# Optimization experiments

Hardware: AMD Instinct MI355X
Metric: run time of the kernel (lower is better)

## Reference

```python
import jax, jax.numpy as jnp
import numpy as np

D_MODEL = 1024
NUM_HEADS = 16
D_K = D_MODEL // NUM_HEADS
D_FF = 4096
THETA = 10000.0
EPS = 1e-5
B, S = 4, 2048


def _trunc_normal(key, shape, fan_in, fan_out):
    std = (2.0 / (fan_in + fan_out)) ** 0.5
    return jax.random.truncated_normal(key, -3.0, 3.0, shape, jnp.float32) * std


def setup_inputs() -> dict:
    key = jax.random.key(0)
    ks = jax.random.split(key, 8)
    return {
        "x": jax.random.normal(ks[0], (B, S, D_MODEL), jnp.float32),
        "wq": _trunc_normal(ks[1], (D_MODEL, D_MODEL), D_MODEL, D_MODEL),
        "wk": _trunc_normal(ks[2], (D_MODEL, D_MODEL), D_MODEL, D_MODEL),
        "wv": _trunc_normal(ks[3], (D_MODEL, D_MODEL), D_MODEL, D_MODEL),
        "wo": _trunc_normal(ks[4], (D_MODEL, D_MODEL), D_MODEL, D_MODEL),
        "g1": jnp.ones((D_MODEL,), jnp.float32),
        "g2": jnp.ones((D_MODEL,), jnp.float32),
        "w1": _trunc_normal(ks[5], (D_FF, D_MODEL), D_MODEL, D_FF),
        "w2": _trunc_normal(ks[6], (D_MODEL, D_FF), D_FF, D_MODEL),
        "w3": _trunc_normal(ks[7], (D_FF, D_MODEL), D_MODEL, D_FF),
    }


def _rmsnorm(x, g):
    rms = jnp.sqrt(jnp.mean(x * x, axis=-1, keepdims=True) + EPS)
    return x / rms * g


def _rope(x):
    # x: [b, h, s, d_k], interleaved rotary embedding
    s = x.shape[-2]
    inv_freq = 1.0 / (THETA ** (jnp.arange(0, D_K, 2, dtype=jnp.float32) / D_K))
    angles = jnp.arange(s, dtype=jnp.float32)[:, None] * inv_freq  # [s, d_k/2]
    cos, sin = jnp.cos(angles), jnp.sin(angles)
    x1, x2 = x[..., ::2], x[..., 1::2]
    rot = jnp.stack([x1 * cos - x2 * sin, x1 * sin + x2 * cos], axis=-1)
    return rot.reshape(x.shape)


def reference(x, wq, wk, wv, wo, g1, g2, w1, w2, w3):
    b, s, _ = x.shape
    h, dk = NUM_HEADS, D_K

    # --- attention sublayer ---
    xn = _rmsnorm(x, g1)
    q = (xn @ wq.T).reshape(b, s, h, dk).transpose(0, 2, 1, 3)
    k = (xn @ wk.T).reshape(b, s, h, dk).transpose(0, 2, 1, 3)
    v = (xn @ wv.T).reshape(b, s, h, dk).transpose(0, 2, 1, 3)
    q, k = _rope(q), _rope(k)

    scores = jnp.einsum("bhqd,bhkd->bhqk", q, k) / (dk ** 0.5)
    causal = jnp.tril(jnp.ones((s, s), dtype=bool))
    scores = jnp.where(causal, scores, -1e9)
    attn = jax.nn.softmax(scores, axis=-1)
    ctx = jnp.einsum("bhqk,bhkd->bhqd", attn, v)
    ctx = ctx.transpose(0, 2, 1, 3).reshape(b, s, h * dk)
    y = x + ctx @ wo.T

    # --- SwiGLU FFN sublayer ---
    yn = _rmsnorm(y, g2)
    a = yn @ w1.T
    ff = (a * jax.nn.sigmoid(a)) * (yn @ w3.T)
    return y + ff @ w2.T
```

## Files before the change

### kernel.cpp

```cpp
#include <hip/hip_runtime.h>
#include <hip/hip_bf16.h>

typedef unsigned short u16;
typedef unsigned int u32;
typedef __bf16 bf16_8 __attribute__((ext_vector_type(8)));
typedef float f32x4 __attribute__((ext_vector_type(4)));

#define DEV __device__ __forceinline__

static const int T_TOK = 8192;
static const int DM    = 1024;
static const int SEQ   = 2048;

DEV u16 f2b(float f) {
  union { float f; u32 u; } v; v.f = f;
  u32 r = v.u + 0x7fffu + ((v.u >> 16) & 1u);
  return (u16)(r >> 16);
}
DEV float b2f(u16 b) {
  union { u32 u; float f; } v; v.u = ((u32)b) << 16;
  return v.f;
}
DEV void gload16(void* lds, const void* g) {
  __builtin_amdgcn_global_load_lds((const __attribute__((address_space(1))) u32*)g,
                                   (__attribute__((address_space(3))) u32*)lds, 16, 0, 0);
}
DEV void vmdrain() { asm volatile("s_waitcnt vmcnt(0)" ::: "memory"); }
DEV uint2 tr_read(u32 addr) {
  uint2 r;
  asm volatile("ds_read_b64_tr_b16 %0, %1" : "=v"(r) : "v"(addr));
  return r;
}

__global__ void cvt_bf16(const float* __restrict__ in, u16* __restrict__ out, int n) {
  int i = (blockIdx.x * blockDim.x + threadIdx.x) * 4;
  if (i >= n) return;
  float4 v = *(const float4*)(in + i);
  union { u16 h[4]; uint2 u; } pk;
  pk.h[0] = f2b(v.x); pk.h[1] = f2b(v.y); pk.h[2] = f2b(v.z); pk.h[3] = f2b(v.w);
  *(uint2*)(out + i) = pk.u;
}

__launch_bounds__(256)
__global__ void rmsnorm_k(const float* __restrict__ x, const float* __restrict__ g,
                          u16* __restrict__ out) {
  const int row = blockIdx.x;
  const float4 v = ((const float4*)(x + (size_t)row * DM))[threadIdx.x];
  float ss = v.x*v.x + v.y*v.y + v.z*v.z + v.w*v.w;
  #pragma unroll
  for (int off = 1; off < 64; off <<= 1) ss += __shfl_xor(ss, off, 64);
  __shared__ float ws[4];
  if ((threadIdx.x & 63) == 0) ws[threadIdx.x >> 6] = ss;
  __syncthreads();
  float tot = ws[0] + ws[1] + ws[2] + ws[3];
  float inv = rsqrtf(tot * (1.0f / DM) + 1e-5f);
  const float4 gv = ((const float4*)g)[threadIdx.x];
  union { u16 h[4]; uint2 u; } pk;
  pk.h[0] = f2b(v.x * inv * gv.x);
  pk.h[1] = f2b(v.y * inv * gv.y);
  pk.h[2] = f2b(v.z * inv * gv.z);
  pk.h[3] = f2b(v.w * inv * gv.w);
  *(uint2*)(out + (size_t)row * DM + threadIdx.x * 4) = pk.u;
}

__global__ void rope_k(u16* __restrict__ buf, float scale) {
  int idx = blockIdx.x * blockDim.x + threadIdx.x;
  if (idx >= T_TOK * 512) return;
  int t = idx >> 9;
  int p = idx & 511;
  int d = p & 31;
  int s = t & (SEQ - 1);
  float inv = __expf(-(float)d * (logf(10000.0f) / 32.0f));
  float ang = (float)s * inv;
  float sn = sinf(ang), cs = cosf(ang);
  size_t off = (size_t)t * DM + (size_t)(p >> 5) * 64 + 2 * d;
  float x1 = b2f(buf[off]), x2 = b2f(buf[off + 1]);
  buf[off]     = f2b((x1 * cs - x2 * sn) * scale);
  buf[off + 1] = f2b((x1 * sn + x2 * cs) * scale);
}


#define GEMM_STAGE(As, Bs, Ap, Bp, K)                                          \
  {                                                                            \
    int c = tid;                                                               \
    gload16((char*)As + (size_t)w * 1024,                                      \
            Ap + (size_t)(brow + (c >> 2)) * K + kk + (((c & 3) ^ ((c >> 3) & 3)) << 3)); \
    gload16((char*)Bs + (size_t)w * 1024,                                      \
            Bp + (size_t)(bcol + (c >> 2)) * K + kk + (((c & 3) ^ ((c >> 3) & 3)) << 3)); \
    c = tid + 256;                                                             \
    gload16((char*)As + 4096 + (size_t)w * 1024,                               \
            Ap + (size_t)(brow + (c >> 2)) * K + kk + (((c & 3) ^ ((c >> 3) & 3)) << 3)); \
    gload16((char*)Bs + 4096 + (size_t)w * 1024,                               \
            Bp + (size_t)(bcol + (c >> 2)) * K + kk + (((c & 3) ^ ((c >> 3) & 3)) << 3)); \
  }

#define GEMM_MFMA(As, Bs)                                                      \
  {                                                                            \
    const int swz = ((lr >> 1) & 3) ^ lg;                                      \
    bf16_8 af[4], bfr[4];                                                      \
    _Pragma("unroll")                                                          \
    for (int m = 0; m < 4; ++m)                                                \
      af[m] = *(const bf16_8*)&As[(wr * 64 + m * 16 + lr) * 32 + (swz << 3)];  \
    _Pragma("unroll")                                                          \
    for (int n = 0; n < 4; ++n)                                                \
      bfr[n] = *(const bf16_8*)&Bs[(wc * 64 + n * 16 + lr) * 32 + (swz << 3)]; \
    _Pragma("unroll")                                                          \
    for (int m = 0; m < 4; ++m)                                                \
      _Pragma("unroll")                                                        \
      for (int n = 0; n < 4; ++n)                                              \
        acc[m][n] = __builtin_amdgcn_mfma_f32_16x16x32_bf16(af[m], bfr[n], acc[m][n], 0, 0, 0); \
  }

template<int MODE>
__launch_bounds__(256)
__global__ void gemm_nt(const u16* __restrict__ A, const u16* __restrict__ B,
                        u16* Cb, float* __restrict__ Cf,
                        const float* __restrict__ resid, const u16* aux,
                        int N, int K) {
  __shared__ __attribute__((aligned(16))) u16 As[128 * 32];
  __shared__ __attribute__((aligned(16))) u16 Bs[128 * 32];
  const int tid = threadIdx.x;
  const int w = tid >> 6, l = tid & 63;
  const int wr = w >> 1, wc = w & 1;
  const int nwg = gridDim.x * gridDim.y;
  const int id  = blockIdx.y * gridDim.x + blockIdx.x;
  const int nid = (id & 7) * (nwg >> 3) + (id >> 3);
  const int bx = nid % gridDim.x, by = nid / gridDim.x;
  const int brow = by * 128;
  const int bcol = bx * 128;
  const int lr = l & 15, lg = l >> 4;
  f32x4 acc[4][4] = {};

  for (int kk = 0; kk < K; kk += 32) {
    GEMM_STAGE(As, Bs, A, B, K)
    vmdrain();
    __syncthreads();
    GEMM_MFMA(As, Bs)
    __syncthreads();
  }

  #pragma unroll
  for (int m = 0; m < 4; ++m) {
    #pragma unroll
    for (int n = 0; n < 4; ++n) {
      #pragma unroll
      for (int r = 0; r < 4; ++r) {
        int row = brow + wr * 64 + m * 16 + lg * 4 + r;
        int col = bcol + wc * 64 + n * 16 + lr;
        size_t idx = (size_t)row * N + col;
        float v = acc[m][n][r];
        if (MODE == 0) {
          Cb[idx] = f2b(v);
        } else if (MODE == 1 || MODE == 3) {
          Cf[idx] = resid[idx] + v;
        } else if (MODE == 2) {
          float av = b2f(aux[idx]);
          float sig = 1.0f / (1.0f + __expf(-av));
          Cb[idx] = f2b(av * sig * v);
        }
      }
    }
  }
}

__launch_bounds__(256)
__global__ void gemm_qkv(const u16* __restrict__ A,
                         const u16* __restrict__ Bq, const u16* __restrict__ Bk,
                         const u16* __restrict__ Bv,
                         u16* __restrict__ Oq, u16* __restrict__ Ok,
                         u16* __restrict__ Ov) {
  __shared__ __attribute__((aligned(16))) u16 As[128 * 32];
  __shared__ __attribute__((aligned(16))) u16 Bs[128 * 32];
  const int tid = threadIdx.x;
  const int w = tid >> 6, l = tid & 63;
  const int wr = w >> 1, wc = w & 1;
  const int nwg = gridDim.x * gridDim.y;
  const int id  = blockIdx.y * gridDim.x + blockIdx.x;
  const int nid = (id & 7) * (nwg >> 3) + (id >> 3);
  const int bx = nid % gridDim.x, by = nid / gridDim.x;
  const int brow = by * 128;
  const int mi = bx >> 3;
  const int bcol = (bx & 7) * 128;
  const u16* B = (mi == 0) ? Bq : (mi == 1) ? Bk : Bv;
  u16* O = (mi == 0) ? Oq : (mi == 1) ? Ok : Ov;
  const int lr = l & 15, lg = l >> 4;
  const int K = 1024;
  f32x4 acc[4][4] = {};

  for (int kk = 0; kk < K; kk += 32) {
    GEMM_STAGE(As, Bs, A, B, K)
    vmdrain();
    __syncthreads();
    GEMM_MFMA(As, Bs)
    __syncthreads();
  }

  #pragma unroll
  for (int m = 0; m < 4; ++m)
    #pragma unroll
    for (int n = 0; n < 4; ++n)
      #pragma unroll
      for (int r = 0; r < 4; ++r) {
        int row = brow + wr * 64 + m * 16 + lg * 4 + r;
        int col = bcol + wc * 64 + n * 16 + lr;
        O[(size_t)row * 1024 + col] = f2b(acc[m][n][r]);
      }
}

__launch_bounds__(256)
__global__ void attn_k(const u16* __restrict__ Q, const u16* __restrict__ Kb,
                       const u16* __restrict__ V, u16* __restrict__ CTX) {
  __shared__ __attribute__((aligned(16))) u16 Ks[64 * 64];
  __shared__ __attribute__((aligned(16))) u16 Vs[64 * 64];
  __shared__ __attribute__((aligned(16))) u16 Ps[4][16 * 64];
  const int tid = threadIdx.x, w = tid >> 6, l = tid & 63;
  const int bh = blockIdx.y;
  const int b = bh >> 4, h = bh & 15;
  const int lr = l & 15, lg = l >> 4;
  const size_t base = (size_t)b * SEQ * DM + (size_t)h * 64;
  const u32 vs_base = (u32)(size_t)&Vs[0];

  #pragma unroll 1
  for (int pass = 0; pass < 2; ++pass) {
    const int qt = pass ? (31 - blockIdx.x) : blockIdx.x;
    const int q0 = qt * 64;

    const size_t qrow = base + (size_t)(q0 + w * 16 + lr) * DM;
    bf16_8 qf0 = *(const bf16_8*)&Q[qrow + lg * 8];
    bf16_8 qf1 = *(const bf16_8*)&Q[qrow + 32 + lg * 8];

    f32x4 o[4] = {};
    float mrow[4], lsum[4];
    #pragma unroll
    for (int r = 0; r < 4; ++r) { mrow[r] = -3.0e38f; lsum[r] = 0.0f; }

    for (int kv0 = 0; kv0 < q0 + 64; kv0 += 64) {
      __syncthreads();
      {
        int u = tid, row = u >> 3, slot = u & 7;
        gload16((char*)Ks + (size_t)w * 1024,
                Kb + base + (size_t)(kv0 + row) * DM + ((slot * 8) ^ ((row & 7) << 3)));
        u = tid + 256; row = u >> 3; slot = u & 7;
        gload16((char*)Ks + 4096 + (size_t)w * 1024,
                Kb + base + (size_t)(kv0 + row) * DM + ((slot * 8) ^ ((row & 7) << 3)));
        u = tid;
        int kv = ((u >> 5) << 2) + ((u >> 1) & 3);
        int d  = (((u >> 3) & 3) << 4) + ((u & 1) << 3);
        gload16((char*)Vs + (size_t)w * 1024,
                V + base + (size_t)(kv0 + kv) * DM + d);
        u = tid + 256;
        kv = ((u >> 5) << 2) + ((u >> 1) & 3);
        d  = (((u >> 3) & 3) << 4) + ((u & 1) << 3);
        gload16((char*)Vs + 4096 + (size_t)w * 1024,
                V + base + (size_t)(kv0 + kv) * DM + d);
      }
      vmdrain();
      __syncthreads();

      f32x4 s[4];
      #pragma unroll
      for (int h0 = 0; h0 < 4; ++h0) {
        const int row = h0 * 16 + lr;
        bf16_8 k0 = *(const bf16_8*)&Ks[row * 64 + ((lg * 8) ^ ((lr & 7) << 3))];
        bf16_8 k1 = *(const bf16_8*)&Ks[row * 64 + ((32 + lg * 8) ^ ((lr & 7) << 3))];
        f32x4 z = {};
        z = __builtin_amdgcn_mfma_f32_16x16x32_bf16(qf0, k0, z, 0, 0, 0);
        z = __builtin_amdgcn_mfma_f32_16x16x32_bf16(qf1, k1, z, 0, 0, 0);
        s[h0] = z;
      }

      #pragma unroll
      for (int r = 0; r < 4; ++r) {
        const int qg = q0 + w * 16 + lg * 4 + r;
        #pragma unroll
        for (int h0 = 0; h0 < 4; ++h0) {
          int kg = kv0 + h0 * 16 + lr;
          if (kg > qg) s[h0][r] = -3.0e38f;
        }
        float vmax = fmaxf(fmaxf(s[0][r], s[1][r]), fmaxf(s[2][r], s[3][r]));
        #pragma unroll
        for (int off = 1; off < 16; off <<= 1) vmax = fmaxf(vmax, __shfl_xor(vmax, off, 64));
        float mnew = fmaxf(mrow[r], vmax);
        float alpha = __expf(mrow[r] - mnew);
        mrow[r] = mnew;
        float p[4], rs = 0.0f;
        #pragma unroll
        for (int h0 = 0; h0 < 4; ++h0) { p[h0] = __expf(s[h0][r] - mnew); rs += p[h0]; }
        #pragma unroll
        for (int off = 1; off < 16; off <<= 1) rs += __shfl_xor(rs, off, 64);
        lsum[r] = lsum[r] * alpha + rs;
        o[0][r] *= alpha; o[1][r] *= alpha; o[2][r] *= alpha; o[3][r] *= alpha;
        const int ql = lg * 4 + r;
        #pragma unroll
        for (int h0 = 0; h0 < 4; ++h0)
          Ps[w][ql * 64 + (((h0 * 16 + lr) ^ ((ql & 7) << 3)))] = f2b(p[h0]);
      }

      #pragma unroll
      for (int kc = 0; kc < 2; ++kc) {
        bf16_8 pf = *(const bf16_8*)&Ps[w][lr * 64 + (((kc * 32 + lg * 8) ^ ((lr & 7) << 3)))];
        uint2 t0[4], t1[4];
        #pragma unroll
        for (int n = 0; n < 4; ++n) {
          u32 a0 = vs_base + (u32)((((kc * 8 + lg * 2 + 0) * 4 + n) * 128) + lr * 8);
          u32 a1 = vs_base + (u32)((((kc * 8 + lg * 2 + 1) * 4 + n) * 128) + lr * 8);
          t0[n] = tr_read(a0);
          t1[n] = tr_read(a1);
        }
        asm volatile("s_waitcnt lgkmcnt(0)" ::: "memory");
        __builtin_amdgcn_sched_barrier(0);
        #pragma unroll
        for (int n = 0; n < 4; ++n) {
          union { uint2 u2[2]; bf16_8 v; } vf;
          vf.u2[0] = t0[n]; vf.u2[1] = t1[n];
          o[n] = __builtin_amdgcn_mfma_f32_16x16x32_bf16(pf, vf.v, o[n], 0, 0, 0);
        }
      }
    }

    #pragma unroll
    for (int r = 0; r < 4; ++r) {
      float inv = 1.0f / lsum[r];
      size_t row = (size_t)b * SEQ + q0 + w * 16 + lg * 4 + r;
      #pragma unroll
      for (int n = 0; n < 4; ++n)
        CTX[row * DM + h * 64 + n * 16 + lr] = f2b(o[n][r] * inv);
    }
  }
}

extern "C" void kernel_launch(void* const* d_in, const int* in_sizes, int n_in,
                              void* d_out, int out_size, void* d_ws, size_t ws_size,
                              hipStream_t stream) {
  const float* x  = (const float*)d_in[0];
  const float* wq = (const float*)d_in[1];
  const float* wk = (const float*)d_in[2];
  const float* wv = (const float*)d_in[3];
  const float* wo = (const float*)d_in[4];
  const float* g1 = (const float*)d_in[5];
  const float* g2 = (const float*)d_in[6];
  const float* w1 = (const float*)d_in[7];
  const float* w2 = (const float*)d_in[8];
  const float* w3 = (const float*)d_in[9];

  char* ws = (char*)d_ws;
  const size_t MB = 1024 * 1024;
  u16*  WQb  = (u16*)(ws +  0 * MB);
  u16*  WKb  = (u16*)(ws +  2 * MB);
  u16*  WVb  = (u16*)(ws +  4 * MB);
  u16*  WOb  = (u16*)(ws +  6 * MB);
  u16*  W1b  = (u16*)(ws +  8 * MB);
  u16*  W3b  = (u16*)(ws + 16 * MB);
  u16*  W2b  = (u16*)(ws + 24 * MB);
  u16*  XN   = (u16*)(ws + 32 * MB);
  u16*  Qb   = (u16*)(ws + 48 * MB);
  u16*  Kb   = (u16*)(ws + 64 * MB);
  u16*  Vb   = (u16*)(ws + 80 * MB);
  u16*  CTX  = (u16*)(ws + 96 * MB);
  float* Y   = (float*)(ws + 112 * MB);
  u16*  FFIN = (u16*)(ws + 48 * MB);

  cvt_bf16<<<1024, 256, 0, stream>>>(wq, WQb, 1048576);
  cvt_bf16<<<1024, 256, 0, stream>>>(wk, WKb, 1048576);
  cvt_bf16<<<1024, 256, 0, stream>>>(wv, WVb, 1048576);
  cvt_bf16<<<1024, 256, 0, stream>>>(wo, WOb, 1048576);
  cvt_bf16<<<4096, 256, 0, stream>>>(w1, W1b, 4194304);
  cvt_bf16<<<4096, 256, 0, stream>>>(w3, W3b, 4194304);
  cvt_bf16<<<4096, 256, 0, stream>>>(w2, W2b, 4194304);

  rmsnorm_k<<<T_TOK, 256, 0, stream>>>(x, g1, XN);

  gemm_qkv<<<dim3(24, 64), 256, 0, stream>>>(XN, WQb, WKb, WVb, Qb, Kb, Vb);

  rope_k<<<16384, 256, 0, stream>>>(Qb, 0.125f);
  rope_k<<<16384, 256, 0, stream>>>(Kb, 1.0f);

  attn_k<<<dim3(16, 64), 256, 0, stream>>>(Qb, Kb, Vb, CTX);

  gemm_nt<1><<<dim3(8, 64), 256, 0, stream>>>(CTX, WOb, nullptr, Y, x, nullptr, 1024, 1024);

  rmsnorm_k<<<T_TOK, 256, 0, stream>>>(Y, g2, XN);

  gemm_nt<0><<<dim3(32, 64), 256, 0, stream>>>(XN, W1b, FFIN, nullptr, nullptr, nullptr, 4096, 1024);
  gemm_nt<2><<<dim3(32, 64), 256, 0, stream>>>(XN, W3b, FFIN, nullptr, nullptr, FFIN, 4096, 1024);

  gemm_nt<3><<<dim3(8, 64), 256, 0, stream>>>(FFIN, W2b, nullptr, (float*)d_out, Y, nullptr, 1024, 4096);
}
```

Measured before the change: 750.5 us.

## Double-buffer GEMM and attention LDS tiles and restructure flash-attention softmax

The GEMM and attention kernels now keep two LDS buffers and prefetch the next K tile while computing on the current one, waiting with vmcnt(4) instead of draining all loads. Attention swaps the QK^T MFMA operands so each lane owns one query row, which cuts the row reductions to two shuffles. It also adds a lazy rescale that skips the alpha update when the running max grows by at most 8, and XCD-aware block remapping. The extra LDS halves potential occupancy, and the lazy rescale relies on bounded exponent growth for accuracy.

```diff
diff --git a/kernel.cpp b/kernel.cpp
--- a/kernel.cpp
+++ b/kernel.cpp
@@ -25,12 +25,15 @@
   __builtin_amdgcn_global_load_lds((const __attribute__((address_space(1))) u32*)g,
                                    (__attribute__((address_space(3))) u32*)lds, 16, 0, 0);
 }
-DEV void vmdrain() { asm volatile("s_waitcnt vmcnt(0)" ::: "memory"); }
 DEV uint2 tr_read(u32 addr) {
   uint2 r;
   asm volatile("ds_read_b64_tr_b16 %0, %1" : "=v"(r) : "v"(addr));
   return r;
 }
+#define VMCNT4 asm volatile("s_waitcnt vmcnt(4)" ::: "memory")
+#define VMCNT0 asm volatile("s_waitcnt vmcnt(0)" ::: "memory")
+#define SBAR   __builtin_amdgcn_s_barrier()
+#define SCHED0 __builtin_amdgcn_sched_barrier(0)
 
 __global__ void cvt_bf16(const float* __restrict__ in, u16* __restrict__ out, int n) {
   int i = (blockIdx.x * blockDim.x + threadIdx.x) * 4;
@@ -80,35 +83,49 @@
 }
 
 
-#define GEMM_STAGE(As, Bs, Ap, Bp, K)                                          \
-  {                                                                            \
-    int c = tid;                                                               \
-    gload16((char*)As + (size_t)w * 1024,                                      \
-            Ap + (size_t)(brow + (c >> 2)) * K + kk + (((c & 3) ^ ((c >> 3) & 3)) << 3)); \
-    gload16((char*)Bs + (size_t)w * 1024,                                      \
-            Bp + (size_t)(bcol + (c >> 2)) * K + kk + (((c & 3) ^ ((c >> 3) & 3)) << 3)); \
-    c = tid + 256;                                                             \
-    gload16((char*)As + 4096 + (size_t)w * 1024,                               \
-            Ap + (size_t)(brow + (c >> 2)) * K + kk + (((c & 3) ^ ((c >> 3) & 3)) << 3)); \
-    gload16((char*)Bs + 4096 + (size_t)w * 1024,                               \
-            Bp + (size_t)(bcol + (c >> 2)) * K + kk + (((c & 3) ^ ((c >> 3) & 3)) << 3)); \
-  }
-
-#define GEMM_MFMA(As, Bs)                                                      \
-  {                                                                            \
-    const int swz = ((lr >> 1) & 3) ^ lg;                                      \
-    bf16_8 af[4], bfr[4];                                                      \
-    _Pragma("unroll")                                                          \
-    for (int m = 0; m < 4; ++m)                                                \
-      af[m] = *(const bf16_8*)&As[(wr * 64 + m * 16 + lr) * 32 + (swz << 3)];  \
-    _Pragma("unroll")                                                          \
-    for (int n = 0; n < 4; ++n)                                                \
-      bfr[n] = *(const bf16_8*)&Bs[(wc * 64 + n * 16 + lr) * 32 + (swz << 3)]; \
-    _Pragma("unroll")                                                          \
-    for (int m = 0; m < 4; ++m)                                                \
-      _Pragma("unroll")                                                        \
-      for (int n = 0; n < 4; ++n)                                              \
+#define GEMM_STAGE(d, kk)                                                       \
+  {                                                                             \
+    int c = tid;                                                                \
+    gload16((char*)As + (d) * 8192 + (size_t)w * 1024,                          \
+            A + (size_t)(brow + (c >> 2)) * K + (kk) + (((c & 3) ^ ((c >> 3) & 3)) << 3)); \
+    gload16((char*)Bs + (d) * 8192 + (size_t)w * 1024,                          \
+            B + (size_t)(bcol + (c >> 2)) * K + (kk) + (((c & 3) ^ ((c >> 3) & 3)) << 3)); \
+    c = tid + 256;                                                              \
+    gload16((char*)As + (d) * 8192 + 4096 + (size_t)w * 1024,                   \
+            A + (size_t)(brow + (c >> 2)) * K + (kk) + (((c & 3) ^ ((c >> 3) & 3)) << 3)); \
+    gload16((char*)Bs + (d) * 8192 + 4096 + (size_t)w * 1024,                   \
+            B + (size_t)(bcol + (c >> 2)) * K + (kk) + (((c & 3) ^ ((c >> 3) & 3)) << 3)); \
+  }
+
+#define GEMM_MFMA(d)                                                            \
+  {                                                                             \
+    const u16* Ab = &As[d][0]; const u16* Bb = &Bs[d][0];                       \
+    const int swz = (((lr >> 1) & 3) ^ lg) << 3;                                \
+    bf16_8 af[4], bfr[4];                                                       \
+    _Pragma("unroll")                                                           \
+    for (int m = 0; m < 4; ++m)                                                 \
+      af[m] = *(const bf16_8*)&Ab[(wr * 64 + m * 16 + lr) * 32 + swz];          \
+    _Pragma("unroll")                                                           \
+    for (int n = 0; n < 4; ++n)                                                 \
+      bfr[n] = *(const bf16_8*)&Bb[(wc * 64 + n * 16 + lr) * 32 + swz];         \
+    _Pragma("unroll")                                                           \
+    for (int m = 0; m < 4; ++m)                                                 \
+      _Pragma("unroll")                                                         \
+      for (int n = 0; n < 4; ++n)                                               \
         acc[m][n] = __builtin_amdgcn_mfma_f32_16x16x32_bf16(af[m], bfr[n], acc[m][n], 0, 0, 0); \
+  }
+
+#define GEMM_LOOP                                                               \
+  const int nt = K >> 5;                                                        \
+  GEMM_STAGE(0, 0)                                                              \
+  int cur = 0;                                                                  \
+  for (int t = 0; t < nt; ++t) {                                                \
+    if (t + 1 < nt) { GEMM_STAGE(cur ^ 1, (t + 1) * 32) VMCNT4; }               \
+    else VMCNT0;                                                                \
+    SBAR; SCHED0;                                                               \
+    GEMM_MFMA(cur)                                                              \
+    SCHED0; SBAR;                                                               \
+    cur ^= 1;                                                                   \
   }
 
 template<int MODE>
@@ -117,8 +134,8 @@
                         u16* Cb, float* __restrict__ Cf,
                         const float* __restrict__ resid, const u16* aux,
                         int N, int K) {
-  __shared__ __attribute__((aligned(16))) u16 As[128 * 32];
-  __shared__ __attribute__((aligned(16))) u16 Bs[128 * 32];
+  __shared__ __attribute__((aligned(16))) u16 As[2][128 * 32];
+  __shared__ __attribute__((aligned(16))) u16 Bs[2][128 * 32];
   const int tid = threadIdx.x;
   const int w = tid >> 6, l = tid & 63;
   const int wr = w >> 1, wc = w & 1;
@@ -131,13 +148,7 @@
   const int lr = l & 15, lg = l >> 4;
   f32x4 acc[4][4] = {};
 
-  for (int kk = 0; kk < K; kk += 32) {
-    GEMM_STAGE(As, Bs, A, B, K)
-    vmdrain();
-    __syncthreads();
-    GEMM_MFMA(As, Bs)
-    __syncthreads();
-  }
+  GEMM_LOOP
 
   #pragma unroll
   for (int m = 0; m < 4; ++m) {
@@ -169,8 +180,8 @@
                          const u16* __restrict__ Bv,
                          u16* __restrict__ Oq, u16* __restrict__ Ok,
                          u16* __restrict__ Ov) {
-  __shared__ __attribute__((aligned(16))) u16 As[128 * 32];
-  __shared__ __attribute__((aligned(16))) u16 Bs[128 * 32];
+  __shared__ __attribute__((aligned(16))) u16 As[2][128 * 32];
+  __shared__ __attribute__((aligned(16))) u16 Bs[2][128 * 32];
   const int tid = threadIdx.x;
   const int w = tid >> 6, l = tid & 63;
   const int wr = w >> 1, wc = w & 1;
@@ -187,13 +198,7 @@
   const int K = 1024;
   f32x4 acc[4][4] = {};
 
-  for (int kk = 0; kk < K; kk += 32) {
-    GEMM_STAGE(As, Bs, A, B, K)
-    vmdrain();
-    __syncthreads();
-    GEMM_MFMA(As, Bs)
-    __syncthreads();
-  }
+  GEMM_LOOP
 
   #pragma unroll
   for (int m = 0; m < 4; ++m)
@@ -210,105 +215,134 @@
 __launch_bounds__(256)
 __global__ void attn_k(const u16* __restrict__ Q, const u16* __restrict__ Kb,
                        const u16* __restrict__ V, u16* __restrict__ CTX) {
-  __shared__ __attribute__((aligned(16))) u16 Ks[64 * 64];
-  __shared__ __attribute__((aligned(16))) u16 Vs[64 * 64];
+  __shared__ __attribute__((aligned(16))) u16 Ks[2][64 * 64];
+  __shared__ __attribute__((aligned(16))) u16 Vs[2][64 * 64];
   __shared__ __attribute__((aligned(16))) u16 Ps[4][16 * 64];
   const int tid = threadIdx.x, w = tid >> 6, l = tid & 63;
-  const int bh = blockIdx.y;
+  const int lr = l & 15, lg = l >> 4;
+  const int id = blockIdx.y * gridDim.x + blockIdx.x;
+  const int xcd = id & 7, slot = id >> 3;
+  const int bh = xcd * 8 + (slot >> 4);
+  const int qx = slot & 15;
   const int b = bh >> 4, h = bh & 15;
-  const int lr = l & 15, lg = l >> 4;
   const size_t base = (size_t)b * SEQ * DM + (size_t)h * 64;
-  const u32 vs_base = (u32)(size_t)&Vs[0];
+  const u32 vs0 = (u32)(size_t)&Vs[0][0];
+
+#define ATT_STAGE(d, kv0)                                                       \
+  {                                                                             \
+    int u = tid, row = u >> 3, sl = u & 7;                                      \
+    gload16((char*)Ks + (d) * 8192 + (size_t)w * 1024,                          \
+            Kb + base + (size_t)((kv0) + row) * DM + ((sl * 8) ^ ((row & 7) << 3))); \
+    u = tid + 256; row = u >> 3; sl = u & 7;                                    \
+    gload16((char*)Ks + (d) * 8192 + 4096 + (size_t)w * 1024,                   \
+            Kb + base + (size_t)((kv0) + row) * DM + ((sl * 8) ^ ((row & 7) << 3))); \
+    u = tid;                                                                    \
+    { int kv = ((u >> 5) << 2) + ((u >> 1) & 3);                                \
+      int dd = (((u >> 3) & 3) << 4) + ((u & 1) << 3);                          \
+      gload16((char*)Vs + (d) * 8192 + (size_t)w * 1024,                        \
+              V + base + (size_t)((kv0) + kv) * DM + dd); }                     \
+    u = tid + 256;                                                              \
+    { int kv = ((u >> 5) << 2) + ((u >> 1) & 3);                                \
+      int dd = (((u >> 3) & 3) << 4) + ((u & 1) << 3);                          \
+      gload16((char*)Vs + (d) * 8192 + 4096 + (size_t)w * 1024,                 \
+              V + base + (size_t)((kv0) + kv) * DM + dd); }                     \
+  }
 
   #pragma unroll 1
   for (int pass = 0; pass < 2; ++pass) {
-    const int qt = pass ? (31 - blockIdx.x) : blockIdx.x;
+    const int qt = pass ? (31 - qx) : qx;
     const int q0 = qt * 64;
-
-    const size_t qrow = base + (size_t)(q0 + w * 16 + lr) * DM;
-    bf16_8 qf0 = *(const bf16_8*)&Q[qrow + lg * 8];
-    bf16_8 qf1 = *(const bf16_8*)&Q[qrow + 32 + lg * 8];
+    const int qg = q0 + w * 16 + lr;
+    const size_t qrow = base + (size_t)qg * DM;
+    const bf16_8 qf0 = *(const bf16_8*)&Q[qrow + lg * 8];
+    const bf16_8 qf1 = *(const bf16_8*)&Q[qrow + 32 + lg * 8];
 
     f32x4 o[4] = {};
-    float mrow[4], lsum[4];
-    #pragma unroll
-    for (int r = 0; r < 4; ++r) { mrow[r] = -3.0e38f; lsum[r] = 0.0f; }
-
-    for (int kv0 = 0; kv0 < q0 + 64; kv0 += 64) {
-      __syncthreads();
-      {
-        int u = tid, row = u >> 3, slot = u & 7;
-        gload16((char*)Ks + (size_t)w * 1024,
-                Kb + base + (size_t)(kv0 + row) * DM + ((slot * 8) ^ ((row & 7) << 3)));
-        u = tid + 256; row = u >> 3; slot = u & 7;
-        gload16((char*)Ks + 4096 + (size_t)w * 1024,
-                Kb + base + (size_t)(kv0 + row) * DM + ((slot * 8) ^ ((row & 7) << 3)));
-        u = tid;
-        int kv = ((u >> 5) << 2) + ((u >> 1) & 3);
-        int d  = (((u >> 3) & 3) << 4) + ((u & 1) << 3);
-        gload16((char*)Vs + (size_t)w * 1024,
-                V + base + (size_t)(kv0 + kv) * DM + d);
-        u = tid + 256;
-        kv = ((u >> 5) << 2) + ((u >> 1) & 3);
-        d  = (((u >> 3) & 3) << 4) + ((u & 1) << 3);
-        gload16((char*)Vs + 4096 + (size_t)w * 1024,
-                V + base + (size_t)(kv0 + kv) * DM + d);
-      }
-      vmdrain();
-      __syncthreads();
+    float mr = -3.0e38f, ls = 0.0f;
+    const int nt = qt + 1;
+    ATT_STAGE(0, 0)
+    int cur = 0;
+
+    for (int t = 0; t < nt; ++t) {
+      const int kv0 = t * 64;
+      if (t + 1 < nt) { ATT_STAGE(cur ^ 1, kv0 + 64) VMCNT4; }
+      else VMCNT0;
+      SBAR; SCHED0;
 
       f32x4 s[4];
+      const u16* kbuf = &Ks[cur][0];
       #pragma unroll
       for (int h0 = 0; h0 < 4; ++h0) {
         const int row = h0 * 16 + lr;
-        bf16_8 k0 = *(const bf16_8*)&Ks[row * 64 + ((lg * 8) ^ ((lr & 7) << 3))];
-        bf16_8 k1 = *(const bf16_8*)&Ks[row * 64 + ((32 + lg * 8) ^ ((lr & 7) << 3))];
+        bf16_8 k0 = *(const bf16_8*)&kbuf[row * 64 + ((lg * 8) ^ ((lr & 7) << 3))];
+        bf16_8 k1 = *(const bf16_8*)&kbuf[row * 64 + ((32 + lg * 8) ^ ((lr & 7) << 3))];
         f32x4 z = {};
-        z = __builtin_amdgcn_mfma_f32_16x16x32_bf16(qf0, k0, z, 0, 0, 0);
-        z = __builtin_amdgcn_mfma_f32_16x16x32_bf16(qf1, k1, z, 0, 0, 0);
+        z = __builtin_amdgcn_mfma_f32_16x16x32_bf16(k0, qf0, z, 0, 0, 0);
+        z = __builtin_amdgcn_mfma_f32_16x16x32_bf16(k1, qf1, z, 0, 0, 0);
         s[h0] = z;
       }
 
-      #pragma unroll
-      for (int r = 0; r < 4; ++r) {
-        const int qg = q0 + w * 16 + lg * 4 + r;
+      if (kv0 + 63 > q0 + w * 16) {
         #pragma unroll
         for (int h0 = 0; h0 < 4; ++h0) {
-          int kg = kv0 + h0 * 16 + lr;
-          if (kg > qg) s[h0][r] = -3.0e38f;
+          int kb = kv0 + h0 * 16 + lg * 4;
+          #pragma unroll
+          for (int r = 0; r < 4; ++r)
+            if (kb + r > qg) s[h0][r] = -3.0e38f;
         }
-        float vmax = fmaxf(fmaxf(s[0][r], s[1][r]), fmaxf(s[2][r], s[3][r]));
+      }
+
+      float pm = s[0][0];
+      #pragma unroll
+      for (int h0 = 0; h0 < 4; ++h0)
         #pragma unroll
-        for (int off = 1; off < 16; off <<= 1) vmax = fmaxf(vmax, __shfl_xor(vmax, off, 64));
-        float mnew = fmaxf(mrow[r], vmax);
-        float alpha = __expf(mrow[r] - mnew);
-        mrow[r] = mnew;
-        float p[4], rs = 0.0f;
+        for (int r = 0; r < 4; ++r) pm = fmaxf(pm, s[h0][r]);
+      pm = fmaxf(pm, __shfl_xor(pm, 16, 64));
+      pm = fmaxf(pm, __shfl_xor(pm, 32, 64));
+
+      if (!__all(pm - mr <= 8.0f)) {
+        float mnew = fmaxf(mr, pm);
+        float alpha = __expf(mr - mnew);
+        mr = mnew;
+        ls *= alpha;
         #pragma unroll
-        for (int h0 = 0; h0 < 4; ++h0) { p[h0] = __expf(s[h0][r] - mnew); rs += p[h0]; }
-        #pragma unroll
-        for (int off = 1; off < 16; off <<= 1) rs += __shfl_xor(rs, off, 64);
-        lsum[r] = lsum[r] * alpha + rs;
-        o[0][r] *= alpha; o[1][r] *= alpha; o[2][r] *= alpha; o[3][r] *= alpha;
-        const int ql = lg * 4 + r;
-        #pragma unroll
-        for (int h0 = 0; h0 < 4; ++h0)
-          Ps[w][ql * 64 + (((h0 * 16 + lr) ^ ((ql & 7) << 3)))] = f2b(p[h0]);
-      }
-
+        for (int r = 0; r < 4; ++r) {
+          float ar = __shfl(alpha, lg * 4 + r, 64);
+          o[0][r] *= ar; o[1][r] *= ar; o[2][r] *= ar; o[3][r] *= ar;
+        }
+      }
+
+      float rs = 0.0f;
+      #pragma unroll
+      for (int h0 = 0; h0 < 4; ++h0) {
+        float p0 = __expf(s[h0][0] - mr);
+        float p1 = __expf(s[h0][1] - mr);
+        float p2 = __expf(s[h0][2] - mr);
+        float p3 = __expf(s[h0][3] - mr);
+        rs += (p0 + p1) + (p2 + p3);
+        union { u16 hh[4]; uint2 u; } pk;
+        pk.hh[0] = f2b(p0); pk.hh[1] = f2b(p1); pk.hh[2] = f2b(p2); pk.hh[3] = f2b(p3);
+        int e = (h0 * 16 + lg * 4) ^ ((lr & 7) << 3);
+        *(uint2*)&Ps[w][lr * 64 + e] = pk.u;
+      }
+      rs += __shfl_xor(rs, 16, 64);
+      rs += __shfl_xor(rs, 32, 64);
+      ls += rs;
+
+      const u32 vb = vs0 + (u32)(cur * 8192);
       #pragma unroll
       for (int kc = 0; kc < 2; ++kc) {
         bf16_8 pf = *(const bf16_8*)&Ps[w][lr * 64 + (((kc * 32 + lg * 8) ^ ((lr & 7) << 3)))];
         uint2 t0[4], t1[4];
         #pragma unroll
         for (int n = 0; n < 4; ++n) {
-          u32 a0 = vs_base + (u32)((((kc * 8 + lg * 2 + 0) * 4 + n) * 128) + lr * 8);
-          u32 a1 = vs_base + (u32)((((kc * 8 + lg * 2 + 1) * 4 + n) * 128) + lr * 8);
+          u32 a0 = vb + (u32)((((kc * 8 + lg * 2 + 0) * 4 + n) * 128) + lr * 8);
+          u32 a1 = vb + (u32)((((kc * 8 + lg * 2 + 1) * 4 + n) * 128) + lr * 8);
           t0[n] = tr_read(a0);
           t1[n] = tr_read(a1);
         }
         asm volatile("s_waitcnt lgkmcnt(0)" ::: "memory");
-        __builtin_amdgcn_sched_barrier(0);
+        SCHED0;
         #pragma unroll
         for (int n = 0; n < 4; ++n) {
           union { uint2 u2[2]; bf16_8 v; } vf;
@@ -316,17 +350,20 @@
           o[n] = __builtin_amdgcn_mfma_f32_16x16x32_bf16(pf, vf.v, o[n], 0, 0, 0);
         }
       }
+      SCHED0; SBAR;
+      cur ^= 1;
     }
 
     #pragma unroll
     for (int r = 0; r < 4; ++r) {
-      float inv = 1.0f / lsum[r];
+      float inv = 1.0f / __shfl(ls, lg * 4 + r, 64);
       size_t row = (size_t)b * SEQ + q0 + w * 16 + lg * 4 + r;
       #pragma unroll
       for (int n = 0; n < 4; ++n)
         CTX[row * DM + h * 64 + n * 16 + lr] = f2b(o[n][r] * inv);
     }
   }
+#undef ATT_STAGE
 }
 
 extern "C" void kernel_launch(void* const* d_in, const int* in_sizes, int n_in,
```

Measured after the change: 672.2 us. 10.4% less time.
